# Kernel tuning notes

Measured on AMD Instinct MI355X. Metric: run time of the kernel, lower is better.

The kernel has to match this reference:

```python
import jax, jax.numpy as jnp
import numpy as np

B, S, D = 2, 1024, 4096
H, KV, HD = 32, 8, 128
GROUP = H // KV


def qlinear(x, w_int8, w_scale, bias):
    """Int8 dynamic-activation-quant linear: per-row activation scale, per-out-channel weight scale."""
    K = x.shape[-1]
    xf = x.reshape(-1, K)
    sx = jnp.max(jnp.abs(xf), axis=1, keepdims=True) / 127.0  # [M,1]
    sx = jnp.where(sx == 0, jnp.float32(1.0), sx)
    xi = jax.lax.stop_gradient(jnp.clip(jnp.round(xf / sx), -127.0, 127.0)).astype(jnp.int8)
    y = jnp.matmul(xi.astype(jnp.int32), w_int8.T.astype(jnp.int32)).astype(jnp.float32)  # int32 accum
    y = y * sx * w_scale[None, :]
    if bias is not None:
        y = y + bias
    return y.reshape(x.shape[:-1] + (w_int8.shape[0],))


def rope(t, c, s):
    half = t.shape[-1] // 2
    rot = jnp.concatenate([-t[..., half:], t[..., :half]], axis=-1)
    return t * c + rot * s


def setup_inputs() -> dict:
    key = jax.random.key(0)
    ks = jax.random.split(key, 10)
    x = jax.random.normal(ks[0], (B, S, D), dtype=jnp.float32)
    # RoPE tables (full-head_dim rotate-half convention)
    inv = 1.0 / (10000.0 ** (jnp.arange(0, HD, 2, dtype=jnp.float32) / HD))
    ang = jnp.arange(S, dtype=jnp.float32)[:, None] * inv[None, :]  # [S, HD/2]
    cos = jnp.concatenate([jnp.cos(ang), jnp.cos(ang)], axis=-1)
    sin = jnp.concatenate([jnp.sin(ang), jnp.sin(ang)], axis=-1)
    d_kv = KV * HD
    wq = jax.random.randint(ks[1], (H * HD, D), -127, 128, dtype=jnp.int32).astype(jnp.int8)
    wk = jax.random.randint(ks[2], (d_kv, D), -127, 128, dtype=jnp.int32).astype(jnp.int8)
    wv = jax.random.randint(ks[3], (d_kv, D), -127, 128, dtype=jnp.int32).astype(jnp.int8)
    wo = jax.random.randint(ks[4], (D, H * HD), -127, 128, dtype=jnp.int32).astype(jnp.int8)
    sc_in = jnp.float32(1.0 / (127.0 * np.sqrt(D)))
    sc_o = jnp.float32(1.0 / (127.0 * np.sqrt(H * HD)))
    sq = jnp.full((H * HD,), sc_in, dtype=jnp.float32)
    sk = jnp.full((d_kv,), sc_in, dtype=jnp.float32)
    sv = jnp.full((d_kv,), sc_in, dtype=jnp.float32)
    so = jnp.full((D,), sc_o, dtype=jnp.float32)
    bq = 0.01 * jax.random.normal(ks[5], (H * HD,), dtype=jnp.float32)
    bk = 0.01 * jax.random.normal(ks[6], (d_kv,), dtype=jnp.float32)
    bv = 0.01 * jax.random.normal(ks[7], (d_kv,), dtype=jnp.float32)
    return {"x": x, "cos": cos, "sin": sin, "wq": wq, "sq": sq, "bq": bq,
            "wk": wk, "sk": sk, "bk": bk, "wv": wv, "sv": sv, "bv": bv,
            "wo": wo, "so": so}


def reference(x, cos, sin, wq, sq, bq, wk, sk, bk, wv, sv, bv, wo, so):
    b, seq, _ = x.shape
    q = qlinear(x, wq, sq, bq).reshape(b, seq, H, HD)
    k = qlinear(x, wk, sk, bk).reshape(b, seq, KV, HD)
    v = qlinear(x, wv, sv, bv).reshape(b, seq, KV, HD)
    c = cos[:seq][None, :, None, :]
    s = sin[:seq][None, :, None, :]
    q = rope(q, c, s)
    k = rope(k, c, s)
    # start_pos=0 prefill: cache write then slice-back is identity -> use k, v directly.
    # GQA broadcast: q_head_to_kv_head = h // group_size
    idx = jnp.arange(H) // GROUP
    kf = k[:, :, idx, :]  # [b, seq, H, HD]
    vf = v[:, :, idx, :]
    scores = jnp.einsum('bqhd,bkhd->bhqk', q, kf) / jnp.sqrt(jnp.float32(HD))
    causal = jnp.tril(jnp.ones((seq, seq), dtype=bool))
    scores = jnp.where(causal[None, None, :, :], scores, jnp.float32(-jnp.inf))
    probs = jax.nn.softmax(scores, axis=-1)
    out = jnp.einsum('bhqk,bkhd->bqhd', probs, vf).reshape(b, seq, H * HD)
    return qlinear(out, wo, so, None)
```

## Files before the change

kernel.cpp:

```cpp
#include <hip/hip_runtime.h>


#define B_   2
#define S_   1024
#define D_   4096
#define H_   32
#define KV_  8
#define HD_  128
#define NR   (B_ * S_)
#define NQKV (H_*HD_ + 2*KV_*HD_)

#define KSTR 132
#define VSTR 68

typedef __attribute__((ext_vector_type(8))) short  short8;
typedef __attribute__((ext_vector_type(4))) float  f32x4;
typedef __attribute__((ext_vector_type(4))) int    int4v;

static __device__ __forceinline__ unsigned short f2bf(float f) {
    unsigned u = __builtin_bit_cast(unsigned, f);
    u += 0x7fffu + ((u >> 16) & 1u);
    return (unsigned short)(u >> 16);
}

static __device__ __forceinline__ void async_cp16(const void* g, void* l) {
    __builtin_amdgcn_global_load_lds(
        (const __attribute__((address_space(1))) void*)g,
        (__attribute__((address_space(3))) void*)l, 16, 0, 0);
}

__global__ __launch_bounds__(256) void quantize_rows_k(
    const float* __restrict__ X, signed char* __restrict__ Xq,
    float* __restrict__ sx_out)
{
    int row = blockIdx.x;
    const f32x4* xr = (const f32x4*)(X + (size_t)row * 4096);
    int t = threadIdx.x;

    f32x4 v[4];
    #pragma unroll
    for (int i = 0; i < 4; i++) v[i] = xr[t + i * 256];

    float m = 0.f;
    #pragma unroll
    for (int i = 0; i < 4; i++)
        #pragma unroll
        for (int j = 0; j < 4; j++) m = fmaxf(m, fabsf(v[i][j]));
    #pragma unroll
    for (int off = 32; off > 0; off >>= 1) m = fmaxf(m, __shfl_down(m, off, 64));
    __shared__ float red[4];
    if ((t & 63) == 0) red[t >> 6] = m;
    __syncthreads();
    float mm = fmaxf(fmaxf(red[0], red[1]), fmaxf(red[2], red[3]));
    float sx = mm / 127.0f;
    if (sx == 0.f) sx = 1.f;
    if (t == 0) sx_out[row] = sx;

    int* dst = (int*)(Xq + (size_t)row * 4096);
    #pragma unroll
    for (int i = 0; i < 4; i++) {
        int o = 0;
        #pragma unroll
        for (int j = 0; j < 4; j++) {
            float q = rintf(v[i][j] / sx);
            q = fminf(fmaxf(q, -127.f), 127.f);
            o |= (((int)q) & 0xff) << (j * 8);
        }
        dst[t + i * 256] = o;
    }
}

__global__ __launch_bounds__(256) void convert_all_w(
    const int* __restrict__ wq, const int* __restrict__ wk,
    const int* __restrict__ wv, const int* __restrict__ wo,
    signed char* __restrict__ Wqkv, signed char* __restrict__ Wo)
{
    int i = blockIdx.x * 256 + threadIdx.x;
    const int* src;
    signed char* dst;
    if (i < 1048576)      { src = wq + (size_t)i * 16;              dst = Wqkv + (size_t)i * 16; }
    else if (i < 1310720) { int j = i - 1048576; src = wk + (size_t)j * 16; dst = Wqkv + 16777216 + (size_t)j * 16; }
    else if (i < 1572864) { int j = i - 1310720; src = wv + (size_t)j * 16; dst = Wqkv + 20971520 + (size_t)j * 16; }
    else                  { int j = i - 1572864; src = wo + (size_t)j * 16; dst = Wo + (size_t)j * 16; }
    const int4v* s4 = (const int4v*)src;
    int4v a = s4[0], b = s4[1], c = s4[2], d = s4[3];
    int4v o;
    o[0] = (a[0]&0xff) | ((a[1]&0xff)<<8) | ((a[2]&0xff)<<16) | ((a[3]&0xff)<<24);
    o[1] = (b[0]&0xff) | ((b[1]&0xff)<<8) | ((b[2]&0xff)<<16) | ((b[3]&0xff)<<24);
    o[2] = (c[0]&0xff) | ((c[1]&0xff)<<8) | ((c[2]&0xff)<<16) | ((c[3]&0xff)<<24);
    o[3] = (d[0]&0xff) | ((d[1]&0xff)<<8) | ((d[2]&0xff)<<16) | ((d[3]&0xff)<<24);
    *(int4v*)dst = o;
}

template<int MODE>
__global__ __launch_bounds__(256) void gemm_i8_k(
    const signed char* __restrict__ A, const signed char* __restrict__ Bm,
    float* __restrict__ C, const float* __restrict__ rs,
    const float* __restrict__ cs, int K, int lda, int ldb, int ldc)
{
    __shared__ __align__(16) signed char As[128 * 64];
    __shared__ __align__(16) signed char Bs[128 * 64];

    int t    = threadIdx.x;
    int m0   = blockIdx.y * 128;
    int n0   = blockIdx.x * 128;
    int lane = t & 63;
    int w    = t >> 6;
    int wm   = (w >> 1) * 64;
    int wn   = (w & 1) * 64;
    int l15  = lane & 15;
    int quad = lane >> 4;

    int4v acc[4][4];
    #pragma unroll
    for (int i = 0; i < 4; i++)
        #pragma unroll
        for (int j = 0; j < 4; j++) { int4v z = {0,0,0,0}; acc[i][j] = z; }

    int srow = t >> 2;
    int scol = (t & 3) * 16;
    signed char* lA0 = As + w * 1024;
    signed char* lA1 = As + 4096 + w * 1024;
    signed char* lB0 = Bs + w * 1024;
    signed char* lB1 = Bs + 4096 + w * 1024;

    for (int k0 = 0; k0 < K; k0 += 64) {
        const signed char* ga = A  + (size_t)(m0 + srow) * lda + k0 + scol;
        const signed char* gb = Bm + (size_t)(n0 + srow) * ldb + k0 + scol;
        async_cp16(ga, lA0);
        async_cp16(ga + (size_t)64 * lda, lA1);
        async_cp16(gb, lB0);
        async_cp16(gb + (size_t)64 * ldb, lB1);
        __syncthreads();

        int4v af[4], bf[4];
        #pragma unroll
        for (int i = 0; i < 4; i++) {
            af[i] = *(const int4v*)&As[(wm + i*16 + l15) * 64 + quad * 16];
            bf[i] = *(const int4v*)&Bs[(wn + i*16 + l15) * 64 + quad * 16];
        }
        #pragma unroll
        for (int i = 0; i < 4; i++)
            #pragma unroll
            for (int j = 0; j < 4; j++)
                acc[i][j] = __builtin_amdgcn_mfma_i32_16x16x64_i8(af[i], bf[j], acc[i][j], 0, 0, 0);
        __syncthreads();
    }

    #pragma unroll
    for (int i = 0; i < 4; i++) {
        #pragma unroll
        for (int j = 0; j < 4; j++) {
            #pragma unroll
            for (int r = 0; r < 4; r++) {
                int row = m0 + wm + i*16 + quad*4 + r;
                int col = n0 + wn + j*16 + l15;
                float v = (float)acc[i][j][r];
                if (MODE == 3) v *= rs[row] * cs[col];
                C[(size_t)row * ldc + col] = v;
            }
        }
    }
}

__global__ __launch_bounds__(256) void derope_k(
    const float* __restrict__ Y, const float* __restrict__ sx,
    const float* __restrict__ sq, const float* __restrict__ bq,
    const float* __restrict__ sk, const float* __restrict__ bk,
    const float* __restrict__ sv, const float* __restrict__ bv,
    const float* __restrict__ cosb, const float* __restrict__ sinb,
    unsigned short* __restrict__ Q, unsigned short* __restrict__ Kb,
    unsigned short* __restrict__ Vt)
{
    const float qs = 0.08838834764831845f;
    int r = blockIdx.x;
    int b = r >> 10;
    int s = r & (S_ - 1);
    float sxr = sx[r];
    const float* yr = Y + (size_t)r * NQKV;
    int t = threadIdx.x;

    for (int p = t; p < H_ * 64; p += 256) {
        int h = p >> 6, d = p & 63;
        int ca = h * HD_ + d;
        float a  = yr[ca]      * sxr * sq[ca]      + bq[ca];
        float b2 = yr[ca + 64] * sxr * sq[ca + 64] + bq[ca + 64];
        float c  = cosb[s * HD_ + d], sn = sinb[s * HD_ + d];
        size_t base = (((size_t)(b * H_ + h)) * S_ + s) * HD_;
        Q[base + d]      = f2bf((a * c - b2 * sn) * qs);
        Q[base + d + 64] = f2bf((b2 * c + a * sn) * qs);
    }
    for (int p = t; p < KV_ * 64; p += 256) {
        int kv = p >> 6, d = p & 63;
        int ci = kv * HD_ + d;
        int ca = H_ * HD_ + ci;
        float a  = yr[ca]      * sxr * sk[ci]      + bk[ci];
        float b2 = yr[ca + 64] * sxr * sk[ci + 64] + bk[ci + 64];
        float c  = cosb[s * HD_ + d], sn = sinb[s * HD_ + d];
        size_t base = (((size_t)(b * KV_ + kv)) * S_ + s) * HD_;
        Kb[base + d]      = f2bf(a * c - b2 * sn);
        Kb[base + d + 64] = f2bf(b2 * c + a * sn);
    }
    for (int p = t; p < KV_ * HD_; p += 256) {
        int kv = p >> 7, d = p & 127;
        int ci = kv * HD_ + d;
        int ca = H_ * HD_ + KV_ * HD_ + ci;
        float v = yr[ca] * sxr * sv[ci] + bv[ci];
        size_t idx = (((size_t)(b * KV_ + kv)) * HD_ + d) * S_ + s;
        Vt[idx] = f2bf(v);
    }
}

__global__ __launch_bounds__(256) void flash_attn_k(
    const unsigned short* __restrict__ Qg,
    const unsigned short* __restrict__ Kg,
    const unsigned short* __restrict__ Vg,
    float* __restrict__ O)
{
    __shared__ __align__(16) unsigned short Ks[64 * KSTR];
    __shared__ __align__(16) unsigned short Vs[HD_ * VSTR];

    int pair = blockIdx.x;
    int qt   = 15 - blockIdx.y;
    int b    = pair >> 5;
    int kv   = (pair & 31) >> 2;

    const unsigned short* Qb = Qg + ((size_t)pair * S_ + qt * 64) * HD_;
    const unsigned short* Kbp = Kg + ((size_t)(b * KV_ + kv)) * (S_ * HD_);
    const unsigned short* Vb = Vg + ((size_t)(b * KV_ + kv)) * (HD_ * S_);

    int t    = threadIdx.x;
    int lane = t & 63;
    int w    = t >> 6;
    int l15  = lane & 15;
    int quad = lane >> 4;

    short8 qf[4];
    #pragma unroll
    for (int ks = 0; ks < 4; ks++)
        qf[ks] = *(const short8*)(Qb + (size_t)(w*16 + l15) * HD_ + ks*32 + quad*8);

    f32x4 oacc[8];
    #pragma unroll
    for (int n = 0; n < 8; n++) { f32x4 z = {0.f,0.f,0.f,0.f}; oacc[n] = z; }
    float mrow[4], lrow[4];
    #pragma unroll
    for (int r = 0; r < 4; r++) { mrow[r] = -1e30f; lrow[r] = 0.f; }

    int kr4 = t >> 4, kc = t & 15;
    int vr4 = t >> 3, vc = t & 7;

    for (int j = 0; j <= qt; ++j) {
        int k0 = j * 64;
        __syncthreads();

        #pragma unroll
        for (int p = 0; p < 4; ++p) {
            int krow = p * 16 + kr4;
            short8 kd = *(const short8*)(Kbp + (size_t)(k0 + krow) * HD_ + kc * 8);
            *(short8*)&Ks[krow * KSTR + kc * 8] = kd;
            int vrow = p * 32 + vr4;
            short8 vd = *(const short8*)(Vb + (size_t)vrow * S_ + k0 + vc * 8);
            *(short8*)&Vs[vrow * VSTR + vc * 8] = vd;
        }
        __syncthreads();

        f32x4 sacc[4];
        #pragma unroll
        for (int n = 0; n < 4; n++) { f32x4 z = {0.f,0.f,0.f,0.f}; sacc[n] = z; }
        #pragma unroll
        for (int n = 0; n < 4; n++) {
            #pragma unroll
            for (int ks = 0; ks < 4; ks++) {
                short8 kf = *(const short8*)&Ks[(n*16 + l15) * KSTR + ks*32 + quad*8];
                sacc[n] = __builtin_amdgcn_mfma_f32_16x16x32_bf16(qf[ks], kf, sacc[n], 0, 0, 0);
            }
        }

        if (j == qt) {
            #pragma unroll
            for (int n = 0; n < 4; n++)
                #pragma unroll
                for (int r = 0; r < 4; r++) {
                    int qrow = w*16 + quad*4 + r;
                    int kcol = n*16 + l15;
                    if (kcol > qrow) sacc[n][r] = -1e30f;
                }
        }

        #pragma unroll
        for (int r = 0; r < 4; r++) {
            float mx = fmaxf(fmaxf(sacc[0][r], sacc[1][r]), fmaxf(sacc[2][r], sacc[3][r]));
            mx = fmaxf(mx, __shfl_xor(mx, 1, 64));
            mx = fmaxf(mx, __shfl_xor(mx, 2, 64));
            mx = fmaxf(mx, __shfl_xor(mx, 4, 64));
            mx = fmaxf(mx, __shfl_xor(mx, 8, 64));
            float mnew = fmaxf(mrow[r], mx);
            float alpha = __expf(mrow[r] - mnew);
            mrow[r] = mnew;
            float s = 0.f;
            #pragma unroll
            for (int n = 0; n < 4; n++) {
                float e = __expf(sacc[n][r] - mnew);
                sacc[n][r] = e;
                s += e;
            }
            s += __shfl_xor(s, 1, 64);
            s += __shfl_xor(s, 2, 64);
            s += __shfl_xor(s, 4, 64);
            s += __shfl_xor(s, 8, 64);
            lrow[r] = lrow[r] * alpha + s;
            #pragma unroll
            for (int n = 0; n < 8; n++) oacc[n][r] *= alpha;
        }

        __syncthreads();

        unsigned short* Ps = Ks;
        #pragma unroll
        for (int n = 0; n < 4; n++)
            #pragma unroll
            for (int r = 0; r < 4; r++)
                Ps[(w*16 + quad*4 + r) * KSTR + n*16 + l15] = f2bf(sacc[n][r]);

        short8 pf[2];
        #pragma unroll
        for (int ks = 0; ks < 2; ks++)
            pf[ks] = *(const short8*)&Ps[(w*16 + l15) * KSTR + ks*32 + quad*8];
        #pragma unroll
        for (int n = 0; n < 8; n++) {
            #pragma unroll
            for (int ks = 0; ks < 2; ks++) {
                short8 vf = *(const short8*)&Vs[(n*16 + l15) * VSTR + ks*32 + quad*8];
                oacc[n] = __builtin_amdgcn_mfma_f32_16x16x32_bf16(pf[ks], vf, oacc[n], 0, 0, 0);
            }
        }
    }

    float* Ob = O + ((size_t)(b * S_ + qt * 64)) * (H_*HD_) + (pair & 31) * HD_;
    #pragma unroll
    for (int r = 0; r < 4; r++) {
        float inv = 1.0f / lrow[r];
        int row = w*16 + quad*4 + r;
        #pragma unroll
        for (int n = 0; n < 8; n++)
            Ob[(size_t)row * (H_*HD_) + n*16 + l15] = oacc[n][r] * inv;
    }
}

extern "C" void kernel_launch(void* const* d_in, const int* in_sizes, int n_in,
                              void* d_out, int out_size, void* d_ws, size_t ws_size,
                              hipStream_t stream)
{
    (void)in_sizes; (void)n_in; (void)out_size; (void)ws_size;
    const float* x    = (const float*)d_in[0];
    const float* cosb = (const float*)d_in[1];
    const float* sinb = (const float*)d_in[2];
    const int*   wq   = (const int*)d_in[3];
    const float* sq   = (const float*)d_in[4];
    const float* bq   = (const float*)d_in[5];
    const int*   wk   = (const int*)d_in[6];
    const float* sk   = (const float*)d_in[7];
    const float* bk   = (const float*)d_in[8];
    const int*   wv   = (const int*)d_in[9];
    const float* sv   = (const float*)d_in[10];
    const float* bv   = (const float*)d_in[11];
    const int*   wo   = (const int*)d_in[12];
    const float* so   = (const float*)d_in[13];
    float* out = (float*)d_out;
    char*  ws  = (char*)d_ws;

    signed char*    Xi   = (signed char*)(ws + 0);
    float*          Y    = (float*)(ws + 8388608ull);
    signed char*    Wqkv = (signed char*)(ws + 58720256ull);
    signed char*    Oi   = (signed char*)(ws + 58720256ull);
    signed char*    Wo   = (signed char*)(ws + 83886080ull);
    unsigned short* Q    = (unsigned short*)(ws + 100663296ull);
    unsigned short* Kb   = (unsigned short*)(ws + 117440512ull);
    unsigned short* Vt   = (unsigned short*)(ws + 121634816ull);
    float*          O    = (float*)(ws + 125829120ull);
    float*          sx   = (float*)(ws + 159383552ull);
    float*          sxo  = (float*)(ws + 159391744ull);

    quantize_rows_k<<<dim3(NR), dim3(256), 0, stream>>>(x, Xi, sx);

    convert_all_w<<<dim3(10240), dim3(256), 0, stream>>>(wq, wk, wv, wo, Wqkv, Wo);

    gemm_i8_k<0><<<dim3(48,16,1), dim3(256), 0, stream>>>(
        Xi, Wqkv, Y, nullptr, nullptr, D_, D_, D_, NQKV);

    derope_k<<<dim3(NR), dim3(256), 0, stream>>>(
        Y, sx, sq, bq, sk, bk, sv, bv, cosb, sinb, Q, Kb, Vt);

    flash_attn_k<<<dim3(64, 16), dim3(256), 0, stream>>>(Q, Kb, Vt, O);

    quantize_rows_k<<<dim3(NR), dim3(256), 0, stream>>>(O, Oi, sxo);

    gemm_i8_k<3><<<dim3(32,16,1), dim3(256), 0, stream>>>(
        Oi, Wo, out, sxo, so, D_, D_, D_, D_);
}
```

Before: 442.7 us.

## Double K tile to 128 and XOR-swizzle LDS layout in int8 GEMM

The int8 GEMM now stages a 128-wide K slice per iteration, which halves the number of barrier pairs per tile, and runs two MFMA sub-steps per staged tile. Shared memory tiles are stored in an XOR-swizzled layout of 16-byte chunks to avoid bank conflicts on fragment reads. LDS use per block doubles to 32KB, which may lower occupancy, and there is still no double buffering.

```diff
diff --git a/kernel.cpp b/kernel.cpp
--- a/kernel.cpp
+++ b/kernel.cpp
@@ -98,8 +98,8 @@
     float* __restrict__ C, const float* __restrict__ rs,
     const float* __restrict__ cs, int K, int lda, int ldb, int ldc)
 {
-    __shared__ __align__(16) signed char As[128 * 64];
-    __shared__ __align__(16) signed char Bs[128 * 64];
+    __shared__ __align__(16) signed char As[128 * 128];
+    __shared__ __align__(16) signed char Bs[128 * 128];
 
     int t    = threadIdx.x;
     int m0   = blockIdx.y * 128;
@@ -117,33 +117,38 @@
         #pragma unroll
         for (int j = 0; j < 4; j++) { int4v z = {0,0,0,0}; acc[i][j] = z; }
 
-    int srow = t >> 2;
-    int scol = (t & 3) * 16;
-    signed char* lA0 = As + w * 1024;
-    signed char* lA1 = As + 4096 + w * 1024;
-    signed char* lB0 = Bs + w * 1024;
-    signed char* lB1 = Bs + 4096 + w * 1024;
-
-    for (int k0 = 0; k0 < K; k0 += 64) {
-        const signed char* ga = A  + (size_t)(m0 + srow) * lda + k0 + scol;
-        const signed char* gb = Bm + (size_t)(n0 + srow) * ldb + k0 + scol;
-        async_cp16(ga, lA0);
-        async_cp16(ga + (size_t)64 * lda, lA1);
-        async_cp16(gb, lB0);
-        async_cp16(gb + (size_t)64 * ldb, lB1);
+    int cw   = w * 64 + lane;
+    int smr  = cw >> 3;
+    int scol = cw & 7;
+
+    for (int k0 = 0; k0 < K; k0 += 128) {
+        #pragma unroll
+        for (int p = 0; p < 4; ++p) {
+            int m  = p * 32 + smr;
+            int kc = scol ^ (m & 7);
+            const signed char* ga = A  + (size_t)(m0 + m) * lda + k0 + kc * 16;
+            const signed char* gb = Bm + (size_t)(n0 + m) * ldb + k0 + kc * 16;
+            async_cp16(ga, As + (p * 256 + w * 64) * 16);
+            async_cp16(gb, Bs + (p * 256 + w * 64) * 16);
+        }
         __syncthreads();
 
-        int4v af[4], bf[4];
-        #pragma unroll
-        for (int i = 0; i < 4; i++) {
-            af[i] = *(const int4v*)&As[(wm + i*16 + l15) * 64 + quad * 16];
-            bf[i] = *(const int4v*)&Bs[(wn + i*16 + l15) * 64 + quad * 16];
-        }
-        #pragma unroll
-        for (int i = 0; i < 4; i++)
-            #pragma unroll
-            for (int j = 0; j < 4; j++)
-                acc[i][j] = __builtin_amdgcn_mfma_i32_16x16x64_i8(af[i], bf[j], acc[i][j], 0, 0, 0);
+        #pragma unroll
+        for (int ks = 0; ks < 2; ks++) {
+            int4v af[4], bf[4];
+            #pragma unroll
+            for (int i = 0; i < 4; i++) {
+                int ra = wm + i*16 + l15;
+                int rb = wn + i*16 + l15;
+                af[i] = *(const int4v*)&As[(ra * 8 + (((ks*4 + quad) ^ (ra & 7)))) * 16];
+                bf[i] = *(const int4v*)&Bs[(rb * 8 + (((ks*4 + quad) ^ (rb & 7)))) * 16];
+            }
+            #pragma unroll
+            for (int i = 0; i < 4; i++)
+                #pragma unroll
+                for (int j = 0; j < 4; j++)
+                    acc[i][j] = __builtin_amdgcn_mfma_i32_16x16x64_i8(af[i], bf[j], acc[i][j], 0, 0, 0);
+        }
         __syncthreads();
     }
 
```

New measurement: 428.5 us. 1.03x faster.
